# Kernel optimization log

Measured on AMD Instinct MI355X. Metric: run time of the kernel, lower is better.

Reference implementation:

```python
import jax, jax.numpy as jnp
import numpy as np

NUM_REL = 20000
NUM_EDGES = 640000
DIM_IN = 128
DIM_OUT = 128
NUM_HEAD = 8
DIM_HID = DIM_OUT // NUM_HEAD
NUM_BIN = 10
NEG_SLOPE = 0.2


def leaky_relu(x):
    return jnp.where(x >= 0, x, NEG_SLOPE * x)


def setup_inputs() -> dict:
    key = jax.random.key(0)
    ks = jax.random.split(key, 8)
    emb_rel = jax.random.normal(ks[0], (NUM_REL, DIM_IN), dtype=jnp.float32)
    head = jax.random.randint(ks[1], (NUM_EDGES, 1), 0, NUM_REL)
    tail = jax.random.randint(ks[2], (NUM_EDGES, 1), 0, NUM_REL)
    bins = jax.random.randint(ks[3], (NUM_EDGES, 1), 0, NUM_BIN)
    relation_triplets = jnp.concatenate([head, tail, bins], axis=-1).astype(jnp.int64)
    # xavier-normal-ish init
    attn_proj_w = jax.random.normal(ks[4], (DIM_OUT, 2 * DIM_IN), dtype=jnp.float32) * (2.0 / np.sqrt(2 * DIM_IN + DIM_OUT))
    attn_proj_b = jnp.zeros((DIM_OUT,), dtype=jnp.float32)
    attn_bin = jax.random.normal(ks[5], (NUM_BIN, NUM_HEAD, 1), dtype=jnp.float32) * 0.3
    attn_vec = jax.random.normal(ks[6], (1, NUM_HEAD, DIM_HID), dtype=jnp.float32) * (2.0 / np.sqrt(NUM_HEAD * DIM_HID))
    aggr_proj_w = jax.random.normal(ks[7], (DIM_OUT, DIM_IN), dtype=jnp.float32) * (2.0 / np.sqrt(DIM_IN + DIM_OUT))
    aggr_proj_b = jnp.zeros((DIM_OUT,), dtype=jnp.float32)
    return {"emb_rel": emb_rel, "relation_triplets": relation_triplets,
            "attn_proj_w": attn_proj_w, "attn_proj_b": attn_proj_b,
            "attn_bin": attn_bin, "attn_vec": attn_vec,
            "aggr_proj_w": aggr_proj_w, "aggr_proj_b": aggr_proj_b}


def reference(emb_rel, relation_triplets, attn_proj_w, attn_proj_b, attn_bin, attn_vec, aggr_proj_w, aggr_proj_b):
    num_rel = emb_rel.shape[0]
    head = relation_triplets[..., 0]
    tail = relation_triplets[..., 1]
    bins = relation_triplets[..., 2]
    # edge gather + concat: [E, 2*dim_in]
    concat = jnp.concatenate([emb_rel[head], emb_rel[tail]], axis=-1)
    proj = concat @ attn_proj_w.T + attn_proj_b  # [E, dim_out]
    proj = leaky_relu(proj).reshape(-1, NUM_HEAD, DIM_HID)
    attn_raw = (proj * attn_vec).sum(axis=-1, keepdims=True) + leaky_relu(attn_bin[bins])  # [E,H,1]
    # per-head-relation segment softmax over edges grouped by head index
    seg_max = jax.ops.segment_max(attn_raw, head, num_segments=num_rel)  # [R,H,1]
    attn_val = jnp.exp(attn_raw - seg_max[head])
    seg_sum = jax.ops.segment_sum(attn_val, head, num_segments=num_rel)  # [R,H,1]
    beta = attn_val / (seg_sum[head] + 1e-16)
    msg = (emb_rel[tail] @ aggr_proj_w.T + aggr_proj_b).reshape(-1, NUM_HEAD, DIM_HID)
    out = jax.ops.segment_sum(beta * msg, head, num_segments=num_rel)  # [R,H,Dh]
    return out.reshape(num_rel, -1)
```

## Files before the change

### kernel.cpp

```cpp
#include <hip/hip_runtime.h>
#include <hip/hip_bf16.h>
#include <cstdint>
#include <cstddef>

#define NUM_REL    20000
#define NUM_EDGES  640000
#define DIM        128
#define NUM_HEAD   8
#define DIM_HID    16
#define NUM_BIN    10
#define CAP        128
#define CNT_STR    16
#define PROJ_BLKS  471
#define SCAT_BLKS  625

using u16 = unsigned short;
using u32 = unsigned int;
typedef __attribute__((ext_vector_type(8))) short bf16x8;
typedef __attribute__((ext_vector_type(4))) float f32x4;

__device__ __forceinline__ float b2f(u16 u) { return __uint_as_float(((u32)u) << 16); }
__device__ __forceinline__ float lo2f(u32 u) { return __uint_as_float(u << 16); }
__device__ __forceinline__ float hi2f(u32 u) { return __uint_as_float(u & 0xffff0000u); }
__device__ __forceinline__ float lrelu(float x) { return fmaxf(x, 0.2f * x); }
__device__ __forceinline__ int clampi(int v, int hi) { return v < 0 ? 0 : (v > hi ? hi : v); }
__device__ __forceinline__ float ldf(const void* p, int f32m, int i)
{ return f32m ? ((const float*)p)[i] : b2f(((const u16*)p)[i]); }
__device__ __forceinline__ u16 f2b(float x)
{ u32 u = __float_as_uint(x); u += 0x7fffu + ((u >> 16) & 1u); return (u16)(u >> 16); }
__device__ __forceinline__ u32 pk2(float a, float b)
{ return (u32)f2b(a) | ((u32)f2b(b) << 16); }

__device__ __forceinline__ void detect_flags(const int* __restrict__ trip,
                                             const u16* __restrict__ emb,
                                             int* sF, int tid)
{
    if (tid < 64) {
        bool odd_zero = (trip[2 * tid + 1] == 0) && (trip[2 * tid + 129] == 0);
        unsigned long long m1 = __ballot(odd_zero);
        int ex = (emb[2 * tid] >> 7) & 0xFF;
        bool inr = (ex >= 110) && (ex <= 136);
        unsigned long long m2 = __ballot(inr);
        if (tid == 0) {
            sF[0] = (~m1 == 0ull) ? 1 : 0;
            sF[1] = (__popcll(m2) >= 32) ? 0 : 1;
        }
    }
    __syncthreads();
}

__global__ __launch_bounds__(256) void k_scatter(
    const int* __restrict__ trip, const void* __restrict__ emb,
    int* __restrict__ cnt, int* __restrict__ bucket)
{
    __shared__ int sF[2];
    const int tid = threadIdx.x;
    detect_flags(trip, (const u16*)emb, sF, tid);
    const int is64 = sF[0];

    const int e0 = (blockIdx.x * 256 + tid) * 4;
    int h[4], t[4], b[4], p[4];
    if (is64) {
        const int4* w = (const int4*)(trip + 6 * e0);
        int4 w0 = w[0], w1 = w[1], w2 = w[2], w3 = w[3], w4 = w[4], w5 = w[5];
        h[0] = w0.x; t[0] = w0.z; b[0] = w1.x;
        h[1] = w1.z; t[1] = w2.x; b[1] = w2.z;
        h[2] = w3.x; t[2] = w3.z; b[2] = w4.x;
        h[3] = w4.z; t[3] = w5.x; b[3] = w5.z;
    } else {
        const int4* w = (const int4*)(trip + 3 * e0);
        int4 w0 = w[0], w1 = w[1], w2 = w[2];
        h[0] = w0.x; t[0] = w0.y; b[0] = w0.z;
        h[1] = w0.w; t[1] = w1.x; b[1] = w1.y;
        h[2] = w1.z; t[2] = w1.w; b[2] = w2.x;
        h[3] = w2.y; t[3] = w2.z; b[3] = w2.w;
    }
    #pragma unroll
    for (int i = 0; i < 4; ++i) {
        h[i] = clampi(h[i], NUM_REL - 1);
        t[i] = clampi(t[i], NUM_REL - 1);
        b[i] = clampi(b[i], NUM_BIN - 1);
    }
    #pragma unroll
    for (int i = 0; i < 4; ++i) p[i] = atomicAdd(&cnt[h[i] * CNT_STR], 1);
    #pragma unroll
    for (int i = 0; i < 4; ++i)
        if (p[i] < CAP) bucket[h[i] * CAP + p[i]] = t[i] | (b[i] << 20);
}

__global__ __launch_bounds__(256) void k_proj(
    const void* __restrict__ emb, const int* __restrict__ trip,
    const void* __restrict__ w_attn, const void* __restrict__ w_aggr,
    const void* __restrict__ b_attn, const void* __restrict__ b_aggr,
    float* __restrict__ A, u16* __restrict__ Bb, u16* __restrict__ Mb)
{
    __shared__ u16 sW[128 * 128];
    __shared__ float sBias[128];
    __shared__ int sF[2];

    const int tid = threadIdx.x;
    detect_flags(trip, (const u16*)emb, sF, tid);
    const int f32m = sF[1];

    const int mt = blockIdx.x / 3, nt = blockIdx.x % 3;
    const int r0 = mt * 128;

    if (tid < 128)
        sBias[tid] = (nt == 0) ? 0.f : ldf((nt == 1) ? b_attn : b_aggr, f32m, tid);

    {
        const void* wsrc = (nt == 2) ? w_aggr : w_attn;
        const int stride = (nt == 2) ? 128 : 256;
        const int koff   = (nt == 1) ? 128 : 0;
        if (f32m) {
            const float* src = (const float*)wsrc;
            #pragma unroll
            for (int i = 0; i < 16; ++i) {
                int f = i * 256 + tid;
                int row = f >> 5, pos = f & 31;
                float4 x = ((const float4*)(src + (size_t)row * stride + koff))[pos];
                int chunk = (pos >> 1) ^ (row & 15);
                *(uint2*)&sW[row * 128 + chunk * 8 + (pos & 1) * 4] =
                    make_uint2(pk2(x.x, x.y), pk2(x.z, x.w));
            }
        } else {
            const u16* src = (const u16*)wsrc;
            #pragma unroll
            for (int i = 0; i < 8; ++i) {
                int f = i * 256 + tid;
                int row = f >> 4, pos = f & 15;
                uint4 x = ((const uint4*)(src + (size_t)row * stride + koff))[pos];
                int chunk = pos ^ (row & 15);
                *(uint4*)&sW[row * 128 + chunk * 8] = x;
            }
        }
    }
    __syncthreads();

    const int lane = tid & 63, wid = tid >> 6;
    const int wm = (wid >> 1) * 64, wn = (wid & 1) * 64;
    const int ln15 = lane & 15, q = lane >> 4;

    int arow[4];
    #pragma unroll
    for (int mi = 0; mi < 4; ++mi) {
        int g = r0 + wm + mi * 16 + ln15;
        arow[mi] = (g < NUM_REL) ? g : (NUM_REL - 1);
    }

    f32x4 acc[4][4] = {};
    #pragma unroll
    for (int kk = 0; kk < 4; ++kk) {
        const int cbase = kk * 4 + q;
        const int kc = cbase * 8;
        bf16x8 a[4], b[4];
        #pragma unroll
        for (int mi = 0; mi < 4; ++mi) {
            if (f32m) {
                const float* er = (const float*)emb + (size_t)arow[mi] * DIM + kc;
                float4 x0 = *(const float4*)er;
                float4 x1 = *(const float4*)(er + 4);
                union { bf16x8 v; u32 u[4]; } cv;
                cv.u[0] = pk2(x0.x, x0.y); cv.u[1] = pk2(x0.z, x0.w);
                cv.u[2] = pk2(x1.x, x1.y); cv.u[3] = pk2(x1.z, x1.w);
                a[mi] = cv.v;
            } else {
                a[mi] = *(const bf16x8*)((const u16*)emb + (size_t)arow[mi] * DIM + kc);
            }
        }
        #pragma unroll
        for (int ni = 0; ni < 4; ++ni) {
            int n = wn + ni * 16 + ln15;
            int c = cbase ^ ln15;
            b[ni] = *(const bf16x8*)&sW[n * 128 + c * 8];
        }
        #pragma unroll
        for (int mi = 0; mi < 4; ++mi)
            #pragma unroll
            for (int ni = 0; ni < 4; ++ni)
                acc[mi][ni] = __builtin_amdgcn_mfma_f32_16x16x32_bf16(
                    a[mi], b[ni], acc[mi][ni], 0, 0, 0);
    }

    #pragma unroll
    for (int mi = 0; mi < 4; ++mi) {
        #pragma unroll
        for (int reg = 0; reg < 4; ++reg) {
            int g = r0 + wm + mi * 16 + q * 4 + reg;
            if (g < NUM_REL) {
                #pragma unroll
                for (int ni = 0; ni < 4; ++ni) {
                    int c = wn + ni * 16 + ln15;
                    float v = acc[mi][ni][reg] + sBias[c];
                    size_t o = (size_t)g * DIM + c;
                    if (nt == 0)      A[o]  = v;
                    else if (nt == 1) Bb[o] = f2b(v);
                    else              Mb[o] = f2b(v);
                }
            }
        }
    }
}

__global__ __launch_bounds__(256, 4) void k_segment(
    const float* __restrict__ A, const u16* __restrict__ Bb,
    const u16* __restrict__ Mb, const void* __restrict__ attn_bin,
    const void* __restrict__ attn_vec, const int* __restrict__ cnt,
    const int* __restrict__ bucket, const int* __restrict__ trip,
    const void* __restrict__ emb, void* __restrict__ out)
{
    __shared__ float sAr[4][DIM];
    __shared__ float sVec[DIM];
    __shared__ float sBin[NUM_BIN * NUM_HEAD];
    __shared__ int sF[2];

    const int tid  = threadIdx.x;
    detect_flags(trip, (const u16*)emb, sF, tid);
    const int f32m = sF[1];

    const int wid  = tid >> 6, lane = tid & 63;
    const int r = blockIdx.x * 4 + wid;
    int nE = cnt[r * CNT_STR]; if (nE > CAP) nE = CAP;
    const int* __restrict__ bk = bucket + r * CAP;

    {
        const float2* ap = (const float2*)(A + (size_t)r * DIM);
        float2 a2 = ap[lane];
        sAr[wid][2 * lane] = a2.x; sAr[wid][2 * lane + 1] = a2.y;
    }
    if (tid < DIM) sVec[tid] = ldf(attn_vec, f32m, tid);
    else if (tid < DIM + NUM_BIN * NUM_HEAD)
        sBin[tid - DIM] = lrelu(ldf(attn_bin, f32m, tid - DIM));
    __syncthreads();

    if (nE == 0) {
        if (f32m) ((float2*)out)[(size_t)r * 64 + lane] = make_float2(0.f, 0.f);
        else      ((u32*)out)[(size_t)r * 64 + lane] = 0;
        return;
    }

    const int el = lane >> 3, hd = lane & 7;
    const int ah = lane >> 3;

    float av[16], vv[16];
    {
        const float4* pA = (const float4*)(&sAr[wid][hd * DIM_HID]);
        const float4* pV = (const float4*)(&sVec[hd * DIM_HID]);
        #pragma unroll
        for (int i = 0; i < 4; ++i) {
            float4 a4 = pA[i], v4 = pV[i];
            av[4*i+0]=a4.x; av[4*i+1]=a4.y; av[4*i+2]=a4.z; av[4*i+3]=a4.w;
            vv[4*i+0]=v4.x; vv[4*i+1]=v4.y; vv[4*i+2]=v4.z; vv[4*i+3]=v4.w;
        }
    }

    const u16* __restrict__ Mbl = Mb + 2 * lane;

    int tba = (el      < nE) ? bk[el]     : 0;
    int tbb = (8 + el  < nE) ? bk[8 + el] : 0;
    int ia = tba & 0xFFFFF, ib = tbb & 0xFFFFF;
    uint4 q0a, q1a, q0b, q1b;
    {
        const uint4* Ba = (const uint4*)(Bb + (size_t)ia * DIM) + hd * 2;
        const uint4* Bc = (const uint4*)(Bb + (size_t)ib * DIM) + hd * 2;
        q0a = Ba[0]; q1a = Ba[1];
        q0b = Bc[0]; q1b = Bc[1];
    }

    float l = 0.f;
    float ax0 = 0.f, ax1 = 0.f, ay0 = 0.f, ay1 = 0.f;

    for (int base = 0; base < nE; base += 16) {
        u32 mm[16];
        #pragma unroll
        for (int k = 0; k < 8; ++k) {
            int tk = __shfl(ia, k * 8);
            mm[k] = *(const u32*)(Mbl + (size_t)tk * DIM);
        }
        #pragma unroll
        for (int k = 0; k < 8; ++k) {
            int tk = __shfl(ib, k * 8);
            mm[8 + k] = *(const u32*)(Mbl + (size_t)tk * DIM);
        }
        const int bsa = (tba >> 20) & 0xF;
        const int bsb = (tbb >> 20) & 0xF;

        int ea_n  = base + 16 + el;
        int eb_n  = base + 24 + el;
        int tba_n = (ea_n < nE) ? bk[ea_n] : 0;
        int tbb_n = (eb_n < nE) ? bk[eb_n] : 0;
        int ia_n  = tba_n & 0xFFFFF, ib_n = tbb_n & 0xFFFFF;
        uint4 q0an, q1an, q0bn, q1bn;
        {
            const uint4* Ban = (const uint4*)(Bb + (size_t)ia_n * DIM) + hd * 2;
            const uint4* Bcn = (const uint4*)(Bb + (size_t)ib_n * DIM) + hd * 2;
            q0an = Ban[0]; q1an = Ban[1];
            q0bn = Bcn[0]; q1bn = Bcn[1];
        }

        float sa0 = sBin[bsa * NUM_HEAD + hd];
        float sb0 = sBin[bsb * NUM_HEAD + hd];
        sa0 = fmaf(lrelu(av[0]  + lo2f(q0a.x)), vv[0],  sa0);
        sb0 = fmaf(lrelu(av[0]  + lo2f(q0b.x)), vv[0],  sb0);
        float sa1 = lrelu(av[1] + hi2f(q0a.x)) * vv[1];
        float sb1 = lrelu(av[1] + hi2f(q0b.x)) * vv[1];
        float sa2 = lrelu(av[2] + lo2f(q0a.y)) * vv[2];
        float sb2 = lrelu(av[2] + lo2f(q0b.y)) * vv[2];
        float sa3 = lrelu(av[3] + hi2f(q0a.y)) * vv[3];
        float sb3 = lrelu(av[3] + hi2f(q0b.y)) * vv[3];
        sa0 = fmaf(lrelu(av[4]  + lo2f(q0a.z)), vv[4],  sa0);
        sb0 = fmaf(lrelu(av[4]  + lo2f(q0b.z)), vv[4],  sb0);
        sa1 = fmaf(lrelu(av[5]  + hi2f(q0a.z)), vv[5],  sa1);
        sb1 = fmaf(lrelu(av[5]  + hi2f(q0b.z)), vv[5],  sb1);
        sa2 = fmaf(lrelu(av[6]  + lo2f(q0a.w)), vv[6],  sa2);
        sb2 = fmaf(lrelu(av[6]  + lo2f(q0b.w)), vv[6],  sb2);
        sa3 = fmaf(lrelu(av[7]  + hi2f(q0a.w)), vv[7],  sa3);
        sb3 = fmaf(lrelu(av[7]  + hi2f(q0b.w)), vv[7],  sb3);
        sa0 = fmaf(lrelu(av[8]  + lo2f(q1a.x)), vv[8],  sa0);
        sb0 = fmaf(lrelu(av[8]  + lo2f(q1b.x)), vv[8],  sb0);
        sa1 = fmaf(lrelu(av[9]  + hi2f(q1a.x)), vv[9],  sa1);
        sb1 = fmaf(lrelu(av[9]  + hi2f(q1b.x)), vv[9],  sb1);
        sa2 = fmaf(lrelu(av[10] + lo2f(q1a.y)), vv[10], sa2);
        sb2 = fmaf(lrelu(av[10] + lo2f(q1b.y)), vv[10], sb2);
        sa3 = fmaf(lrelu(av[11] + hi2f(q1a.y)), vv[11], sa3);
        sb3 = fmaf(lrelu(av[11] + hi2f(q1b.y)), vv[11], sb3);
        sa0 = fmaf(lrelu(av[12] + lo2f(q1a.z)), vv[12], sa0);
        sb0 = fmaf(lrelu(av[12] + lo2f(q1b.z)), vv[12], sb0);
        sa1 = fmaf(lrelu(av[13] + hi2f(q1a.z)), vv[13], sa1);
        sb1 = fmaf(lrelu(av[13] + hi2f(q1b.z)), vv[13], sb1);
        sa2 = fmaf(lrelu(av[14] + lo2f(q1a.w)), vv[14], sa2);
        sb2 = fmaf(lrelu(av[14] + lo2f(q1b.w)), vv[14], sb2);
        sa3 = fmaf(lrelu(av[15] + hi2f(q1a.w)), vv[15], sa3);
        sb3 = fmaf(lrelu(av[15] + hi2f(q1b.w)), vv[15], sb3);
        float sa = (sa0 + sa1) + (sa2 + sa3);
        float sb = (sb0 + sb1) + (sb2 + sb3);
        sa = fminf(fmaxf(sa, -60.f), 60.f);
        sb = fminf(fmaxf(sb, -60.f), 60.f);
        float pa = ((base + el)     < nE) ? __expf(sa) : 0.f;
        float pb = ((base + 8 + el) < nE) ? __expf(sb) : 0.f;
        l += pa + pb;

        #pragma unroll
        for (int k = 0; k < 8; ++k) {
            float v = __shfl(pa, k * 8 + ah);
            if (k & 1) { ax1 = fmaf(v, lo2f(mm[k]), ax1); ay1 = fmaf(v, hi2f(mm[k]), ay1); }
            else       { ax0 = fmaf(v, lo2f(mm[k]), ax0); ay0 = fmaf(v, hi2f(mm[k]), ay0); }
        }
        #pragma unroll
        for (int k = 0; k < 8; ++k) {
            float v = __shfl(pb, k * 8 + ah);
            if (k & 1) { ax1 = fmaf(v, lo2f(mm[8+k]), ax1); ay1 = fmaf(v, hi2f(mm[8+k]), ay1); }
            else       { ax0 = fmaf(v, lo2f(mm[8+k]), ax0); ay0 = fmaf(v, hi2f(mm[8+k]), ay0); }
        }

        tba = tba_n; tbb = tbb_n; ia = ia_n; ib = ib_n;
        q0a = q0an; q1a = q1an; q0b = q0bn; q1b = q1bn;
    }

    float accx = ax0 + ax1, accy = ay0 + ay1;

    float lt = l + __shfl_xor(l, 8);
    lt += __shfl_xor(lt, 16);
    lt += __shfl_xor(lt, 32);
    float lA = __shfl(lt, ah);
    float inv = 1.0f / (lA + 1e-16f);
    float o0 = accx * inv, o1 = accy * inv;
    if (f32m) {
        ((float2*)out)[(size_t)r * 64 + lane] = make_float2(o0, o1);
    } else {
        u32 pk = (u32)f2b(o0) | ((u32)f2b(o1) << 16);
        ((u32*)out)[(size_t)r * 64 + lane] = pk;
    }
}

extern "C" void kernel_launch(void* const* d_in, const int* in_sizes, int n_in,
                              void* d_out, int out_size, void* d_ws, size_t ws_size,
                              hipStream_t stream)
{
    (void)in_sizes; (void)n_in; (void)out_size; (void)ws_size;
    const void* emb      = d_in[0];
    const int*  trip     = (const int*)d_in[1];
    const void* w_attn   = d_in[2];
    const void* b_attn   = d_in[3];
    const void* attn_bin = d_in[4];
    const void* attn_vec = d_in[5];
    const void* w_aggr   = d_in[6];
    const void* b_aggr   = d_in[7];

    char* p = (char*)d_ws;
    float* A      = (float*)p; p += (size_t)NUM_REL * DIM * 4;
    u16*   Bb     = (u16*)p;   p += (size_t)NUM_REL * DIM * 2;
    u16*   Mb     = (u16*)p;   p += (size_t)NUM_REL * DIM * 2;
    int*   bucket = (int*)p;   p += (size_t)NUM_REL * CAP * 4;
    int*   cnt    = (int*)p;   p += (size_t)NUM_REL * CNT_STR * 4;

    hipMemsetAsync(cnt, 0, (size_t)NUM_REL * CNT_STR * sizeof(int), stream);
    k_scatter<<<SCAT_BLKS, 256, 0, stream>>>(trip, emb, cnt, bucket);
    k_proj<<<PROJ_BLKS, 256, 0, stream>>>(
        emb, trip, w_attn, w_aggr, b_attn, b_aggr, A, Bb, Mb);
    k_segment<<<NUM_REL / 4, 256, 0, stream>>>(A, Bb, Mb, attn_bin, attn_vec,
                                               cnt, bucket, trip, emb, d_out);
}
```

Before: 169.4 us.

## Fuse scatter into projection kernel and interleave B/M rows per head

Merges the edge-scatter kernel into the projection kernel as extra blocks, which removes one launch and lets the atomics overlap with the GEMM. The projection weight tile in shared memory is halved and loaded in two K-halves, raising occupancy at the cost of an extra barrier. The B and M projections are written into one interleaved buffer laid out per head, so each lane loads its tail's B and M slices as contiguous 16-byte vectors. Each lane then accumulates 16 output channels per head, replacing per-edge shuffles with a final cross-lane reduction and a store from one lane group.

```diff
diff --git a/kernel.cpp b/kernel.cpp
--- a/kernel.cpp
+++ b/kernel.cpp
@@ -49,58 +49,52 @@
     __syncthreads();
 }
 
-__global__ __launch_bounds__(256) void k_scatter(
-    const int* __restrict__ trip, const void* __restrict__ emb,
-    int* __restrict__ cnt, int* __restrict__ bucket)
-{
-    __shared__ int sF[2];
-    const int tid = threadIdx.x;
-    detect_flags(trip, (const u16*)emb, sF, tid);
-    const int is64 = sF[0];
-
-    const int e0 = (blockIdx.x * 256 + tid) * 4;
-    int h[4], t[4], b[4], p[4];
-    if (is64) {
-        const int4* w = (const int4*)(trip + 6 * e0);
-        int4 w0 = w[0], w1 = w[1], w2 = w[2], w3 = w[3], w4 = w[4], w5 = w[5];
-        h[0] = w0.x; t[0] = w0.z; b[0] = w1.x;
-        h[1] = w1.z; t[1] = w2.x; b[1] = w2.z;
-        h[2] = w3.x; t[2] = w3.z; b[2] = w4.x;
-        h[3] = w4.z; t[3] = w5.x; b[3] = w5.z;
-    } else {
-        const int4* w = (const int4*)(trip + 3 * e0);
-        int4 w0 = w[0], w1 = w[1], w2 = w[2];
-        h[0] = w0.x; t[0] = w0.y; b[0] = w0.z;
-        h[1] = w0.w; t[1] = w1.x; b[1] = w1.y;
-        h[2] = w1.z; t[2] = w1.w; b[2] = w2.x;
-        h[3] = w2.y; t[3] = w2.z; b[3] = w2.w;
-    }
-    #pragma unroll
-    for (int i = 0; i < 4; ++i) {
-        h[i] = clampi(h[i], NUM_REL - 1);
-        t[i] = clampi(t[i], NUM_REL - 1);
-        b[i] = clampi(b[i], NUM_BIN - 1);
-    }
-    #pragma unroll
-    for (int i = 0; i < 4; ++i) p[i] = atomicAdd(&cnt[h[i] * CNT_STR], 1);
-    #pragma unroll
-    for (int i = 0; i < 4; ++i)
-        if (p[i] < CAP) bucket[h[i] * CAP + p[i]] = t[i] | (b[i] << 20);
-}
-
-__global__ __launch_bounds__(256) void k_proj(
+__global__ __launch_bounds__(256) void k_projscatter(
     const void* __restrict__ emb, const int* __restrict__ trip,
     const void* __restrict__ w_attn, const void* __restrict__ w_aggr,
     const void* __restrict__ b_attn, const void* __restrict__ b_aggr,
-    float* __restrict__ A, u16* __restrict__ Bb, u16* __restrict__ Mb)
+    float* __restrict__ A, u16* __restrict__ BM,
+    int* __restrict__ cnt, int* __restrict__ bucket)
 {
-    __shared__ u16 sW[128 * 128];
+    __shared__ u16 sW[128 * 64];
     __shared__ float sBias[128];
     __shared__ int sF[2];
 
     const int tid = threadIdx.x;
     detect_flags(trip, (const u16*)emb, sF, tid);
-    const int f32m = sF[1];
+    const int is64 = sF[0], f32m = sF[1];
+
+    if (blockIdx.x >= PROJ_BLKS) {
+        const int e0 = ((blockIdx.x - PROJ_BLKS) * 256 + tid) * 4;
+        int h[4], t[4], b[4], p[4];
+        if (is64) {
+            const int4* w = (const int4*)(trip + 6 * e0);
+            int4 w0 = w[0], w1 = w[1], w2 = w[2], w3 = w[3], w4 = w[4], w5 = w[5];
+            h[0] = w0.x; t[0] = w0.z; b[0] = w1.x;
+            h[1] = w1.z; t[1] = w2.x; b[1] = w2.z;
+            h[2] = w3.x; t[2] = w3.z; b[2] = w4.x;
+            h[3] = w4.z; t[3] = w5.x; b[3] = w5.z;
+        } else {
+            const int4* w = (const int4*)(trip + 3 * e0);
+            int4 w0 = w[0], w1 = w[1], w2 = w[2];
+            h[0] = w0.x; t[0] = w0.y; b[0] = w0.z;
+            h[1] = w0.w; t[1] = w1.x; b[1] = w1.y;
+            h[2] = w1.z; t[2] = w1.w; b[2] = w2.x;
+            h[3] = w2.y; t[3] = w2.z; b[3] = w2.w;
+        }
+        #pragma unroll
+        for (int i = 0; i < 4; ++i) {
+            h[i] = clampi(h[i], NUM_REL - 1);
+            t[i] = clampi(t[i], NUM_REL - 1);
+            b[i] = clampi(b[i], NUM_BIN - 1);
+        }
+        #pragma unroll
+        for (int i = 0; i < 4; ++i) p[i] = atomicAdd(&cnt[h[i] * CNT_STR], 1);
+        #pragma unroll
+        for (int i = 0; i < 4; ++i)
+            if (p[i] < CAP) bucket[h[i] * CAP + p[i]] = t[i] | (b[i] << 20);
+        return;
+    }
 
     const int mt = blockIdx.x / 3, nt = blockIdx.x % 3;
     const int r0 = mt * 128;
@@ -108,34 +102,9 @@
     if (tid < 128)
         sBias[tid] = (nt == 0) ? 0.f : ldf((nt == 1) ? b_attn : b_aggr, f32m, tid);
 
-    {
-        const void* wsrc = (nt == 2) ? w_aggr : w_attn;
-        const int stride = (nt == 2) ? 128 : 256;
-        const int koff   = (nt == 1) ? 128 : 0;
-        if (f32m) {
-            const float* src = (const float*)wsrc;
-            #pragma unroll
-            for (int i = 0; i < 16; ++i) {
-                int f = i * 256 + tid;
-                int row = f >> 5, pos = f & 31;
-                float4 x = ((const float4*)(src + (size_t)row * stride + koff))[pos];
-                int chunk = (pos >> 1) ^ (row & 15);
-                *(uint2*)&sW[row * 128 + chunk * 8 + (pos & 1) * 4] =
-                    make_uint2(pk2(x.x, x.y), pk2(x.z, x.w));
-            }
-        } else {
-            const u16* src = (const u16*)wsrc;
-            #pragma unroll
-            for (int i = 0; i < 8; ++i) {
-                int f = i * 256 + tid;
-                int row = f >> 4, pos = f & 15;
-                uint4 x = ((const uint4*)(src + (size_t)row * stride + koff))[pos];
-                int chunk = pos ^ (row & 15);
-                *(uint4*)&sW[row * 128 + chunk * 8] = x;
-            }
-        }
-    }
-    __syncthreads();
+    const void* wsrc = (nt == 2) ? w_aggr : w_attn;
+    const int stride = (nt == 2) ? 128 : 256;
+    const int koff   = (nt == 1) ? 128 : 0;
 
     const int lane = tid & 63, wid = tid >> 6;
     const int wm = (wid >> 1) * 64, wn = (wid & 1) * 64;
@@ -150,36 +119,66 @@
 
     f32x4 acc[4][4] = {};
     #pragma unroll
-    for (int kk = 0; kk < 4; ++kk) {
-        const int cbase = kk * 4 + q;
-        const int kc = cbase * 8;
-        bf16x8 a[4], b[4];
-        #pragma unroll
-        for (int mi = 0; mi < 4; ++mi) {
-            if (f32m) {
-                const float* er = (const float*)emb + (size_t)arow[mi] * DIM + kc;
-                float4 x0 = *(const float4*)er;
-                float4 x1 = *(const float4*)(er + 4);
-                union { bf16x8 v; u32 u[4]; } cv;
-                cv.u[0] = pk2(x0.x, x0.y); cv.u[1] = pk2(x0.z, x0.w);
-                cv.u[2] = pk2(x1.x, x1.y); cv.u[3] = pk2(x1.z, x1.w);
-                a[mi] = cv.v;
-            } else {
-                a[mi] = *(const bf16x8*)((const u16*)emb + (size_t)arow[mi] * DIM + kc);
-            }
-        }
-        #pragma unroll
-        for (int ni = 0; ni < 4; ++ni) {
-            int n = wn + ni * 16 + ln15;
-            int c = cbase ^ ln15;
-            b[ni] = *(const bf16x8*)&sW[n * 128 + c * 8];
-        }
-        #pragma unroll
-        for (int mi = 0; mi < 4; ++mi)
-            #pragma unroll
-            for (int ni = 0; ni < 4; ++ni)
-                acc[mi][ni] = __builtin_amdgcn_mfma_f32_16x16x32_bf16(
-                    a[mi], b[ni], acc[mi][ni], 0, 0, 0);
+    for (int kh = 0; kh < 2; ++kh) {
+        if (kh) __syncthreads();
+        if (f32m) {
+            const float* src = (const float*)wsrc;
+            #pragma unroll
+            for (int i = 0; i < 8; ++i) {
+                int f = i * 256 + tid;
+                int row = f >> 4, pos = f & 15;
+                const float* rp = src + (size_t)row * stride + koff + kh * 64;
+                float4 x = ((const float4*)rp)[pos];
+                int chunk = (pos >> 1) ^ (row & 7);
+                *(uint2*)&sW[row * 64 + chunk * 8 + (pos & 1) * 4] =
+                    make_uint2(pk2(x.x, x.y), pk2(x.z, x.w));
+            }
+        } else {
+            const u16* src = (const u16*)wsrc;
+            #pragma unroll
+            for (int i = 0; i < 4; ++i) {
+                int f = i * 256 + tid;
+                int row = f >> 3, pos = f & 7;
+                const u16* rp = src + (size_t)row * stride + koff + kh * 64;
+                uint4 x = ((const uint4*)rp)[pos];
+                int chunk = pos ^ (row & 7);
+                *(uint4*)&sW[row * 64 + chunk * 8] = x;
+            }
+        }
+        __syncthreads();
+
+        #pragma unroll
+        for (int k2 = 0; k2 < 2; ++k2) {
+            const int kkg = kh * 2 + k2;
+            const int kc = (kkg * 4 + q) * 8;
+            const int cl = (k2 * 4 + q) ^ (ln15 & 7);
+            bf16x8 a[4], b[4];
+            #pragma unroll
+            for (int mi = 0; mi < 4; ++mi) {
+                if (f32m) {
+                    const float* er = (const float*)emb + (size_t)arow[mi] * DIM + kc;
+                    float4 x0 = *(const float4*)er;
+                    float4 x1 = *(const float4*)(er + 4);
+                    union { bf16x8 v; u32 u[4]; } cv;
+                    cv.u[0] = pk2(x0.x, x0.y); cv.u[1] = pk2(x0.z, x0.w);
+                    cv.u[2] = pk2(x1.x, x1.y); cv.u[3] = pk2(x1.z, x1.w);
+                    a[mi] = cv.v;
+                } else {
+                    a[mi] = *(const bf16x8*)((const u16*)emb + (size_t)arow[mi] * DIM + kc);
+                }
+            }
+            #pragma unroll
+            for (int ni = 0; ni < 4; ++ni) {
+                int n = wn + ni * 16 + ln15;
+                b[ni] = *(const bf16x8*)&sW[n * 64 + cl * 8];
+            }
+            #pragma unroll
+            for (int mi = 0; mi < 4; ++mi)
+                #pragma unroll
+                for (int ni = 0; ni < 4; ++ni)
+                    acc[mi][ni] = __builtin_amdgcn_mfma_f32_16x16x32_bf16(
+                        a[mi], b[ni], acc[mi][ni], 0, 0, 0);
+        }
     }
 
     #pragma unroll
@@ -192,10 +191,13 @@
                 for (int ni = 0; ni < 4; ++ni) {
                     int c = wn + ni * 16 + ln15;
                     float v = acc[mi][ni][reg] + sBias[c];
-                    size_t o = (size_t)g * DIM + c;
-                    if (nt == 0)      A[o]  = v;
-                    else if (nt == 1) Bb[o] = f2b(v);
-                    else              Mb[o] = f2b(v);
+                    if (nt == 0) {
+                        A[(size_t)g * DIM + c] = v;
+                    } else {
+                        size_t o = (size_t)g * 256 + (size_t)((c >> 4) * 32)
+                                 + (c & 15) + (nt == 2 ? 16 : 0);
+                        BM[o] = f2b(v);
+                    }
                 }
             }
         }
@@ -203,11 +205,11 @@
 }
 
 __global__ __launch_bounds__(256, 4) void k_segment(
-    const float* __restrict__ A, const u16* __restrict__ Bb,
-    const u16* __restrict__ Mb, const void* __restrict__ attn_bin,
-    const void* __restrict__ attn_vec, const int* __restrict__ cnt,
-    const int* __restrict__ bucket, const int* __restrict__ trip,
-    const void* __restrict__ emb, void* __restrict__ out)
+    const float* __restrict__ A, const u16* __restrict__ BM,
+    const void* __restrict__ attn_bin, const void* __restrict__ attn_vec,
+    const int* __restrict__ cnt, const int* __restrict__ bucket,
+    const int* __restrict__ trip, const void* __restrict__ emb,
+    void* __restrict__ out)
 {
     __shared__ float sAr[4][DIM];
     __shared__ float sVec[DIM];
@@ -240,7 +242,6 @@
     }
 
     const int el = lane >> 3, hd = lane & 7;
-    const int ah = lane >> 3;
 
     float av[16], vv[16];
     {
@@ -254,33 +255,31 @@
         }
     }
 
-    const u16* __restrict__ Mbl = Mb + 2 * lane;
+    const u16* __restrict__ BMh = BM + hd * 32;
 
     int tba = (el      < nE) ? bk[el]     : 0;
     int tbb = (8 + el  < nE) ? bk[8 + el] : 0;
     int ia = tba & 0xFFFFF, ib = tbb & 0xFFFFF;
-    uint4 q0a, q1a, q0b, q1b;
+    uint4 qa0, qa1, qb0, qb1;
     {
-        const uint4* Ba = (const uint4*)(Bb + (size_t)ia * DIM) + hd * 2;
-        const uint4* Bc = (const uint4*)(Bb + (size_t)ib * DIM) + hd * 2;
-        q0a = Ba[0]; q1a = Ba[1];
-        q0b = Bc[0]; q1b = Bc[1];
+        const uint4* Ba = (const uint4*)(BMh + (size_t)ia * 256);
+        const uint4* Bc = (const uint4*)(BMh + (size_t)ib * 256);
+        qa0 = Ba[0]; qa1 = Ba[1];
+        qb0 = Bc[0]; qb1 = Bc[1];
     }
 
     float l = 0.f;
-    float ax0 = 0.f, ax1 = 0.f, ay0 = 0.f, ay1 = 0.f;
+    float acc[16];
+    #pragma unroll
+    for (int j = 0; j < 16; ++j) acc[j] = 0.f;
 
     for (int base = 0; base < nE; base += 16) {
-        u32 mm[16];
-        #pragma unroll
-        for (int k = 0; k < 8; ++k) {
-            int tk = __shfl(ia, k * 8);
-            mm[k] = *(const u32*)(Mbl + (size_t)tk * DIM);
-        }
-        #pragma unroll
-        for (int k = 0; k < 8; ++k) {
-            int tk = __shfl(ib, k * 8);
-            mm[8 + k] = *(const u32*)(Mbl + (size_t)tk * DIM);
+        uint4 ma0, ma1, mb0, mb1;
+        {
+            const uint4* Ma = (const uint4*)(BMh + (size_t)ia * 256 + 16);
+            const uint4* Mc = (const uint4*)(BMh + (size_t)ib * 256 + 16);
+            ma0 = Ma[0]; ma1 = Ma[1];
+            mb0 = Mc[0]; mb1 = Mc[1];
         }
         const int bsa = (tba >> 20) & 0xF;
         const int bsb = (tbb >> 20) & 0xF;
@@ -290,48 +289,48 @@
         int tba_n = (ea_n < nE) ? bk[ea_n] : 0;
         int tbb_n = (eb_n < nE) ? bk[eb_n] : 0;
         int ia_n  = tba_n & 0xFFFFF, ib_n = tbb_n & 0xFFFFF;
-        uint4 q0an, q1an, q0bn, q1bn;
+        uint4 qa0n, qa1n, qb0n, qb1n;
         {
-            const uint4* Ban = (const uint4*)(Bb + (size_t)ia_n * DIM) + hd * 2;
-            const uint4* Bcn = (const uint4*)(Bb + (size_t)ib_n * DIM) + hd * 2;
-            q0an = Ban[0]; q1an = Ban[1];
-            q0bn = Bcn[0]; q1bn = Bcn[1];
+            const uint4* Ban = (const uint4*)(BMh + (size_t)ia_n * 256);
+            const uint4* Bcn = (const uint4*)(BMh + (size_t)ib_n * 256);
+            qa0n = Ban[0]; qa1n = Ban[1];
+            qb0n = Bcn[0]; qb1n = Bcn[1];
         }
 
         float sa0 = sBin[bsa * NUM_HEAD + hd];
         float sb0 = sBin[bsb * NUM_HEAD + hd];
-        sa0 = fmaf(lrelu(av[0]  + lo2f(q0a.x)), vv[0],  sa0);
-        sb0 = fmaf(lrelu(av[0]  + lo2f(q0b.x)), vv[0],  sb0);
-        float sa1 = lrelu(av[1] + hi2f(q0a.x)) * vv[1];
-        float sb1 = lrelu(av[1] + hi2f(q0b.x)) * vv[1];
-        float sa2 = lrelu(av[2] + lo2f(q0a.y)) * vv[2];
-        float sb2 = lrelu(av[2] + lo2f(q0b.y)) * vv[2];
-        float sa3 = lrelu(av[3] + hi2f(q0a.y)) * vv[3];
-        float sb3 = lrelu(av[3] + hi2f(q0b.y)) * vv[3];
-        sa0 = fmaf(lrelu(av[4]  + lo2f(q0a.z)), vv[4],  sa0);
-        sb0 = fmaf(lrelu(av[4]  + lo2f(q0b.z)), vv[4],  sb0);
-        sa1 = fmaf(lrelu(av[5]  + hi2f(q0a.z)), vv[5],  sa1);
-        sb1 = fmaf(lrelu(av[5]  + hi2f(q0b.z)), vv[5],  sb1);
-        sa2 = fmaf(lrelu(av[6]  + lo2f(q0a.w)), vv[6],  sa2);
-        sb2 = fmaf(lrelu(av[6]  + lo2f(q0b.w)), vv[6],  sb2);
-        sa3 = fmaf(lrelu(av[7]  + hi2f(q0a.w)), vv[7],  sa3);
-        sb3 = fmaf(lrelu(av[7]  + hi2f(q0b.w)), vv[7],  sb3);
-        sa0 = fmaf(lrelu(av[8]  + lo2f(q1a.x)), vv[8],  sa0);
-        sb0 = fmaf(lrelu(av[8]  + lo2f(q1b.x)), vv[8],  sb0);
-        sa1 = fmaf(lrelu(av[9]  + hi2f(q1a.x)), vv[9],  sa1);
-        sb1 = fmaf(lrelu(av[9]  + hi2f(q1b.x)), vv[9],  sb1);
-        sa2 = fmaf(lrelu(av[10] + lo2f(q1a.y)), vv[10], sa2);
-        sb2 = fmaf(lrelu(av[10] + lo2f(q1b.y)), vv[10], sb2);
-        sa3 = fmaf(lrelu(av[11] + hi2f(q1a.y)), vv[11], sa3);
-        sb3 = fmaf(lrelu(av[11] + hi2f(q1b.y)), vv[11], sb3);
-        sa0 = fmaf(lrelu(av[12] + lo2f(q1a.z)), vv[12], sa0);
-        sb0 = fmaf(lrelu(av[12] + lo2f(q1b.z)), vv[12], sb0);
-        sa1 = fmaf(lrelu(av[13] + hi2f(q1a.z)), vv[13], sa1);
-        sb1 = fmaf(lrelu(av[13] + hi2f(q1b.z)), vv[13], sb1);
-        sa2 = fmaf(lrelu(av[14] + lo2f(q1a.w)), vv[14], sa2);
-        sb2 = fmaf(lrelu(av[14] + lo2f(q1b.w)), vv[14], sb2);
-        sa3 = fmaf(lrelu(av[15] + hi2f(q1a.w)), vv[15], sa3);
-        sb3 = fmaf(lrelu(av[15] + hi2f(q1b.w)), vv[15], sb3);
+        sa0 = fmaf(lrelu(av[0]  + lo2f(qa0.x)), vv[0],  sa0);
+        sb0 = fmaf(lrelu(av[0]  + lo2f(qb0.x)), vv[0],  sb0);
+        float sa1 = lrelu(av[1] + hi2f(qa0.x)) * vv[1];
+        float sb1 = lrelu(av[1] + hi2f(qb0.x)) * vv[1];
+        float sa2 = lrelu(av[2] + lo2f(qa0.y)) * vv[2];
+        float sb2 = lrelu(av[2] + lo2f(qb0.y)) * vv[2];
+        float sa3 = lrelu(av[3] + hi2f(qa0.y)) * vv[3];
+        float sb3 = lrelu(av[3] + hi2f(qb0.y)) * vv[3];
+        sa0 = fmaf(lrelu(av[4]  + lo2f(qa0.z)), vv[4],  sa0);
+        sb0 = fmaf(lrelu(av[4]  + lo2f(qb0.z)), vv[4],  sb0);
+        sa1 = fmaf(lrelu(av[5]  + hi2f(qa0.z)), vv[5],  sa1);
+        sb1 = fmaf(lrelu(av[5]  + hi2f(qb0.z)), vv[5],  sb1);
+        sa2 = fmaf(lrelu(av[6]  + lo2f(qa0.w)), vv[6],  sa2);
+        sb2 = fmaf(lrelu(av[6]  + lo2f(qb0.w)), vv[6],  sb2);
+        sa3 = fmaf(lrelu(av[7]  + hi2f(qa0.w)), vv[7],  sa3);
+        sb3 = fmaf(lrelu(av[7]  + hi2f(qb0.w)), vv[7],  sb3);
+        sa0 = fmaf(lrelu(av[8]  + lo2f(qa1.x)), vv[8],  sa0);
+        sb0 = fmaf(lrelu(av[8]  + lo2f(qb1.x)), vv[8],  sb0);
+        sa1 = fmaf(lrelu(av[9]  + hi2f(qa1.x)), vv[9],  sa1);
+        sb1 = fmaf(lrelu(av[9]  + hi2f(qb1.x)), vv[9],  sb1);
+        sa2 = fmaf(lrelu(av[10] + lo2f(qa1.y)), vv[10], sa2);
+        sb2 = fmaf(lrelu(av[10] + lo2f(qb1.y)), vv[10], sb2);
+        sa3 = fmaf(lrelu(av[11] + hi2f(qa1.y)), vv[11], sa3);
+        sb3 = fmaf(lrelu(av[11] + hi2f(qb1.y)), vv[11], sb3);
+        sa0 = fmaf(lrelu(av[12] + lo2f(qa1.z)), vv[12], sa0);
+        sb0 = fmaf(lrelu(av[12] + lo2f(qb1.z)), vv[12], sb0);
+        sa1 = fmaf(lrelu(av[13] + hi2f(qa1.z)), vv[13], sa1);
+        sb1 = fmaf(lrelu(av[13] + hi2f(qb1.z)), vv[13], sb1);
+        sa2 = fmaf(lrelu(av[14] + lo2f(qa1.w)), vv[14], sa2);
+        sb2 = fmaf(lrelu(av[14] + lo2f(qb1.w)), vv[14], sb2);
+        sa3 = fmaf(lrelu(av[15] + hi2f(qa1.w)), vv[15], sa3);
+        sb3 = fmaf(lrelu(av[15] + hi2f(qb1.w)), vv[15], sb3);
         float sa = (sa0 + sa1) + (sa2 + sa3);
         float sb = (sb0 + sb1) + (sb2 + sb3);
         sa = fminf(fmaxf(sa, -60.f), 60.f);
@@ -340,36 +339,59 @@
         float pb = ((base + 8 + el) < nE) ? __expf(sb) : 0.f;
         l += pa + pb;
 
-        #pragma unroll
-        for (int k = 0; k < 8; ++k) {
-            float v = __shfl(pa, k * 8 + ah);
-            if (k & 1) { ax1 = fmaf(v, lo2f(mm[k]), ax1); ay1 = fmaf(v, hi2f(mm[k]), ay1); }
-            else       { ax0 = fmaf(v, lo2f(mm[k]), ax0); ay0 = fmaf(v, hi2f(mm[k]), ay0); }
-        }
-        #pragma unroll
-        for (int k = 0; k < 8; ++k) {
-            float v = __shfl(pb, k * 8 + ah);
-            if (k & 1) { ax1 = fmaf(v, lo2f(mm[8+k]), ax1); ay1 = fmaf(v, hi2f(mm[8+k]), ay1); }
-            else       { ax0 = fmaf(v, lo2f(mm[8+k]), ax0); ay0 = fmaf(v, hi2f(mm[8+k]), ay0); }
+        {
+            const u32* wa = (const u32*)&ma0;
+            const u32* wb = (const u32*)&mb0;
+            #pragma unroll
+            for (int j = 0; j < 4; ++j) {
+                acc[2*j]   = fmaf(pa, lo2f(wa[j]), acc[2*j]);
+                acc[2*j+1] = fmaf(pa, hi2f(wa[j]), acc[2*j+1]);
+                acc[2*j]   = fmaf(pb, lo2f(wb[j]), acc[2*j]);
+                acc[2*j+1] = fmaf(pb, hi2f(wb[j]), acc[2*j+1]);
+            }
+            const u32* xa = (const u32*)&ma1;
+            const u32* xb = (const u32*)&mb1;
+            #pragma unroll
+            for (int j = 0; j < 4; ++j) {
+                acc[8+2*j]   = fmaf(pa, lo2f(xa[j]), acc[8+2*j]);
+                acc[8+2*j+1] = fmaf(pa, hi2f(xa[j]), acc[8+2*j+1]);
+                acc[8+2*j]   = fmaf(pb, lo2f(xb[j]), acc[8+2*j]);
+                acc[8+2*j+1] = fmaf(pb, hi2f(xb[j]), acc[8+2*j+1]);
+            }
         }
 
         tba = tba_n; tbb = tbb_n; ia = ia_n; ib = ib_n;
-        q0a = q0an; q1a = q1an; q0b = q0bn; q1b = q1bn;
-    }
-
-    float accx = ax0 + ax1, accy = ay0 + ay1;
+        qa0 = qa0n; qa1 = qa1n; qb0 = qb0n; qb1 = qb1n;
+    }
 
     float lt = l + __shfl_xor(l, 8);
     lt += __shfl_xor(lt, 16);
     lt += __shfl_xor(lt, 32);
-    float lA = __shfl(lt, ah);
-    float inv = 1.0f / (lA + 1e-16f);
-    float o0 = accx * inv, o1 = accy * inv;
-    if (f32m) {
-        ((float2*)out)[(size_t)r * 64 + lane] = make_float2(o0, o1);
-    } else {
-        u32 pk = (u32)f2b(o0) | ((u32)f2b(o1) << 16);
-        ((u32*)out)[(size_t)r * 64 + lane] = pk;
+    float inv = 1.0f / (lt + 1e-16f);
+
+    #pragma unroll
+    for (int j = 0; j < 16; ++j) {
+        float v = acc[j];
+        v += __shfl_xor(v, 8);
+        v += __shfl_xor(v, 16);
+        v += __shfl_xor(v, 32);
+        acc[j] = v * inv;
+    }
+
+    if (el == 0) {
+        if (f32m) {
+            float* op = (float*)out + (size_t)r * DIM + hd * DIM_HID;
+            #pragma unroll
+            for (int j = 0; j < 4; ++j) {
+                float4 v4 = make_float4(acc[4*j], acc[4*j+1], acc[4*j+2], acc[4*j+3]);
+                ((float4*)op)[j] = v4;
+            }
+        } else {
+            u32* op = (u32*)out + (size_t)r * 64 + hd * 8;
+            #pragma unroll
+            for (int j = 0; j < 8; ++j)
+                op[j] = pk2(acc[2*j], acc[2*j+1]);
+        }
     }
 }
 
@@ -389,15 +411,13 @@
 
     char* p = (char*)d_ws;
     float* A      = (float*)p; p += (size_t)NUM_REL * DIM * 4;
-    u16*   Bb     = (u16*)p;   p += (size_t)NUM_REL * DIM * 2;
-    u16*   Mb     = (u16*)p;   p += (size_t)NUM_REL * DIM * 2;
+    u16*   BM     = (u16*)p;   p += (size_t)NUM_REL * 256 * 2;
     int*   bucket = (int*)p;   p += (size_t)NUM_REL * CAP * 4;
     int*   cnt    = (int*)p;   p += (size_t)NUM_REL * CNT_STR * 4;
 
     hipMemsetAsync(cnt, 0, (size_t)NUM_REL * CNT_STR * sizeof(int), stream);
-    k_scatter<<<SCAT_BLKS, 256, 0, stream>>>(trip, emb, cnt, bucket);
-    k_proj<<<PROJ_BLKS, 256, 0, stream>>>(
-        emb, trip, w_attn, w_aggr, b_attn, b_aggr, A, Bb, Mb);
-    k_segment<<<NUM_REL / 4, 256, 0, stream>>>(A, Bb, Mb, attn_bin, attn_vec,
+    k_projscatter<<<PROJ_BLKS + SCAT_BLKS, 256, 0, stream>>>(
+        emb, trip, w_attn, w_aggr, b_attn, b_aggr, A, BM, cnt, bucket);
+    k_segment<<<NUM_REL / 4, 256, 0, stream>>>(A, BM, attn_bin, attn_vec,
                                                cnt, bucket, trip, emb, d_out);
 }
```

Result: faster. 163.5 us (-3.5%).
